# Optimization experiments

Measured on AMD Instinct MI355X. Metric: run time of the kernel, lower is better.

The kernel has to match this reference:

```python
import jax, jax.numpy as jnp
import numpy as np

NUM_EMBED = 204
HEAD_DIM = 64
B, T = 4, 4096


def setup_inputs() -> dict:
    key = jax.random.key(0)
    kx, kq, kk, kv = jax.random.split(key, 4)
    x = jax.random.normal(kx, (B, T, NUM_EMBED), dtype=jnp.float32)
    s = 1.0 / np.sqrt(NUM_EMBED)
    Wq = jax.random.normal(kq, (NUM_EMBED, HEAD_DIM), dtype=jnp.float32) * s
    Wk = jax.random.normal(kk, (NUM_EMBED, HEAD_DIM), dtype=jnp.float32) * s
    Wv = jax.random.normal(kv, (NUM_EMBED, HEAD_DIM), dtype=jnp.float32) * s
    return {"x": x, "Wq": Wq, "Wk": Wk, "Wv": Wv, "mask": True}


def reference(x, Wq, Wk, Wv, mask):
    # Single-head causal attention. d_k = x.shape[-1] (as in the source, which
    # scales by sqrt of the INPUT embed dim, not head_dim).
    Bn, Tn, d_k = x.shape
    q = x @ Wq  # [B,T,H]
    k = x @ Wk  # [B,T,H]
    v = x @ Wv  # [B,T,H]
    scale = 1.0 / jnp.sqrt(jnp.asarray(d_k, dtype=x.dtype))
    scores = jnp.einsum("bqh,bkh->bqk", q, k) * scale  # [B,T,T]
    if mask:
        causal = jnp.tril(jnp.ones((Tn, Tn), dtype=bool))  # allow j <= i
        scores = jnp.where(causal, scores, jnp.finfo(scores.dtype).min)
    attn = jax.nn.softmax(scores, axis=-1)
    out = jnp.einsum("bqk,bkh->bqh", attn, v)  # [B,T,H]
    # dropout is identity in eval mode
    return out
```

## Files before the change

kernel.cpp:

```cpp
#include <hip/hip_runtime.h>

#define TSEQ   4096
#define NB     4
#define EMB    204
#define HD     64
#define WK     224
#define XSTR   232
#define PSTR   68
#define KTILE  64

typedef __attribute__((ext_vector_type(8))) short bf16x8;
typedef __attribute__((ext_vector_type(4))) float f32x4;

__device__ __forceinline__ short f2bf(float f) {
    unsigned u = __float_as_uint(f);
    return (short)((u + 0x7fffu + ((u >> 16) & 1u)) >> 16);
}
__device__ __forceinline__ float bf2f(short h) {
    return __uint_as_float(((unsigned)(unsigned short)h) << 16);
}

__global__ __launch_bounds__(256) void prep_zero_kernel(
    const float* __restrict__ Wq,
    const float* __restrict__ Wk,
    const float* __restrict__ Wv,
    short* __restrict__ Wt,
    float* __restrict__ zacc)
{
    int f = blockIdx.x * 256 + threadIdx.x;
    if (f < 3 * HD * WK) {
        int e   = f % WK;
        int h   = (f / WK) % HD;
        int mat = f / (WK * HD);
        const float* W = (mat == 0) ? Wq : (mat == 1) ? Wk : Wv;
        float v = (e < EMB) ? W[e * HD + h] : 0.f;
        Wt[f] = f2bf(v);
    }
    for (int c = blockIdx.x * 256 + threadIdx.x; c < 266240; c += 256 * 256)
        *(float4*)(zacc + c * 4) = make_float4(0.f, 0.f, 0.f, 0.f);
}

__global__ __launch_bounds__(192) void qkv_mfma_kernel(
    const float* __restrict__ x,
    const short* __restrict__ Wt,
    short* __restrict__ qg,
    short* __restrict__ kg,
    short* __restrict__ vtg)
{
    __shared__ __align__(16) short xs[16 * XSTR];

    const int t    = threadIdx.x;
    const int lane = t & 63;
    const int w    = t >> 6;
    const int l15  = lane & 15;
    const int quad = lane >> 4;
    const long long rowb = (long long)blockIdx.x * 16;

    for (int c = t; c < 816; c += 192) {
        int r = c / 51, c4 = c % 51;
        float4 xv = *(const float4*)(x + (rowb + r) * EMB + c4 * 4);
        unsigned p0 = (unsigned)(unsigned short)f2bf(xv.x)
                    | ((unsigned)(unsigned short)f2bf(xv.y) << 16);
        unsigned p1 = (unsigned)(unsigned short)f2bf(xv.z)
                    | ((unsigned)(unsigned short)f2bf(xv.w) << 16);
        uint2 pk; pk.x = p0; pk.y = p1;
        *(uint2*)(&xs[r * XSTR + c4 * 4]) = pk;
    }
    for (int c = t; c < 16 * 28; c += 192) {
        int r = c / 28, cc = c % 28;
        xs[r * XSTR + EMB + cc] = 0;
    }
    __syncthreads();

    f32x4 acc[4];
#pragma unroll
    for (int nt = 0; nt < 4; ++nt) acc[nt] = (f32x4){0.f, 0.f, 0.f, 0.f};

    const short* Wb = Wt + (size_t)w * HD * WK;
#pragma unroll
    for (int ks = 0; ks < 7; ++ks) {
        bf16x8 af = *(const bf16x8*)(&xs[l15 * XSTR + ks * 32 + quad * 8]);
#pragma unroll
        for (int nt = 0; nt < 4; ++nt) {
            bf16x8 bfr = *(const bf16x8*)(Wb + (size_t)(nt * 16 + l15) * WK
                                          + ks * 32 + quad * 8);
            acc[nt] = __builtin_amdgcn_mfma_f32_16x16x32_bf16(af, bfr, acc[nt], 0, 0, 0);
        }
    }

    const float scale = 0.07001400420f;
    if (w == 0) {
#pragma unroll
        for (int r = 0; r < 4; ++r) {
            long long grow = rowb + quad * 4 + r;
#pragma unroll
            for (int nt = 0; nt < 4; ++nt)
                qg[grow * HD + nt * 16 + l15] = f2bf(acc[nt][r] * scale);
        }
    } else if (w == 1) {
#pragma unroll
        for (int r = 0; r < 4; ++r) {
            long long grow = rowb + quad * 4 + r;
#pragma unroll
            for (int nt = 0; nt < 4; ++nt)
                kg[grow * HD + nt * 16 + l15] = f2bf(acc[nt][r]);
        }
    } else {
#pragma unroll
        for (int r = 0; r < 4; ++r) {
            long long grow = rowb + quad * 4 + r;
            int bb = (int)(grow >> 12);
            int tt = (int)(grow & 4095);
#pragma unroll
            for (int nt = 0; nt < 4; ++nt)
                vtg[((long long)bb * HD + nt * 16 + l15) * TSEQ + tt] = f2bf(acc[nt][r]);
        }
    }
}

__global__ __launch_bounds__(256, 3) void flash_mfma_kernel(
    const short* __restrict__ qg,
    const short* __restrict__ kg,
    const short* __restrict__ vtg,
    float* __restrict__ outacc,
    float* __restrict__ lacc)
{
    __shared__ __align__(16) short Ks[2][KTILE * HD];
    __shared__ __align__(16) short Vt[2][HD * KTILE];
    __shared__ __align__(16) short Ps[4 * 32 * PSTR];

    const int t    = threadIdx.x;
    const int lane = t & 63;
    const int w    = t >> 6;
    const int l15  = lane & 15;
    const int quad = lane >> 4;
    const int wq   = w * 32;

    const int b = blockIdx.y;
    const int p = 143 - (int)blockIdx.x;

    int g = 0;
    while (g < 7 && p >= 2 * (g + 1) * (g + 2)) ++g;
    const int rel    = p - 2 * g * (g + 1);
    const int s      = g + 1;
    const int qt3    = 4 * g + rel / s;
    const int split  = rel % s;
    const int ntiles = 2 * qt3 + 2;
    const int chunk  = (ntiles + s - 1) / s;
    const int kt0    = split * chunk;
    const int kt1    = min(ntiles, kt0 + chunk);
    if (kt0 >= kt1) return;

    const int qbase = qt3 * 128;
    const long long rowb = (long long)b * TSEQ;

    bf16x8 aq[2][2];
#pragma unroll
    for (int m = 0; m < 2; ++m)
#pragma unroll
        for (int ss = 0; ss < 2; ++ss)
            aq[m][ss] = *(const bf16x8*)(qg + (rowb + qbase + wq + m * 16 + l15) * HD
                                         + ss * 32 + quad * 8);

    f32x4 Oacc[2][4];
#pragma unroll
    for (int m = 0; m < 2; ++m)
#pragma unroll
        for (int nt = 0; nt < 4; ++nt) Oacc[m][nt] = (f32x4){0.f, 0.f, 0.f, 0.f};
    float lsum[2][4] = {{0.f, 0.f, 0.f, 0.f}, {0.f, 0.f, 0.f, 0.f}};

    short* pw = &Ps[w * 32 * PSTR];

#define STAGE(BUF, KT) do {                                                   \
        const int k0s = (KT) * KTILE;                                         \
        _Pragma("unroll")                                                     \
        for (int j = 0; j < 2; ++j) {                                         \
            const int rr = (w * 2 + j) * 8 + (lane >> 3);                     \
            const int cc = (lane & 7) ^ (rr & 7);                             \
            const short* srcK = kg + (rowb + k0s + rr) * HD + cc * 8;         \
            __builtin_amdgcn_global_load_lds(                                 \
                (const __attribute__((address_space(1))) void*)srcK,          \
                (__attribute__((address_space(3))) void*)&Ks[BUF][(w * 2 + j) * 512], \
                16, 0, 0);                                                    \
            const short* srcV = vtg + ((long long)b * HD + rr) * TSEQ + k0s + cc * 8; \
            __builtin_amdgcn_global_load_lds(                                 \
                (const __attribute__((address_space(1))) void*)srcV,          \
                (__attribute__((address_space(3))) void*)&Vt[BUF][(w * 2 + j) * 512], \
                16, 0, 0);                                                    \
        }                                                                     \
    } while (0)

    int cur = 0;
    STAGE(0, kt0);
    __syncthreads();

    for (int kt = kt0; kt < kt1; ++kt) {
        const int k0 = kt * KTILE;
        if (kt + 1 < kt1) STAGE(cur ^ 1, kt + 1);

        const short* ksb = Ks[cur];
        const short* vsb = Vt[cur];
        const bool act = (k0 <= qbase + wq);

        if (act) {
#pragma unroll
            for (int m = 0; m < 2; ++m) {
                const int rbase = qbase + wq + m * 16;
                f32x4 S[4];
#pragma unroll
                for (int nt = 0; nt < 4; ++nt) S[nt] = (f32x4){0.f, 0.f, 0.f, 0.f};
#pragma unroll
                for (int ss = 0; ss < 2; ++ss) {
#pragma unroll
                    for (int nt = 0; nt < 4; ++nt) {
                        const int rr = nt * 16 + l15;
                        const int cc = ((ss * 4 + quad) ^ (rr & 7)) * 8;
                        bf16x8 bk = *(const bf16x8*)(ksb + rr * HD + cc);
                        S[nt] = __builtin_amdgcn_mfma_f32_16x16x32_bf16(aq[m][ss], bk, S[nt], 0, 0, 0);
                    }
                }
                if (k0 + 63 <= rbase) {
#pragma unroll
                    for (int r = 0; r < 4; ++r) {
#pragma unroll
                        for (int nt = 0; nt < 4; ++nt) {
                            float pv = __expf(S[nt][r]);
                            short h = f2bf(pv);
                            pw[(m * 16 + quad * 4 + r) * PSTR + nt * 16 + l15] = h;
                            lsum[m][r] += bf2f(h);
                        }
                    }
                } else {
#pragma unroll
                    for (int r = 0; r < 4; ++r) {
                        const int irow = rbase + quad * 4 + r;
#pragma unroll
                        for (int nt = 0; nt < 4; ++nt) {
                            const int j = k0 + nt * 16 + l15;
                            float pv = (j <= irow) ? __expf(S[nt][r]) : 0.f;
                            short h = f2bf(pv);
                            pw[(m * 16 + quad * 4 + r) * PSTR + nt * 16 + l15] = h;
                            lsum[m][r] += bf2f(h);
                        }
                    }
                }
            }

#pragma unroll
            for (int ss = 0; ss < 2; ++ss) {
                bf16x8 pa0 = *(const bf16x8*)(pw + l15 * PSTR + ss * 32 + quad * 8);
                bf16x8 pa1 = *(const bf16x8*)(pw + (16 + l15) * PSTR + ss * 32 + quad * 8);
#pragma unroll
                for (int nt = 0; nt < 4; ++nt) {
                    const int hh = nt * 16 + l15;
                    const int cc = ((ss * 4 + quad) ^ (hh & 7)) * 8;
                    bf16x8 vb = *(const bf16x8*)(vsb + hh * HD + cc);
                    Oacc[0][nt] = __builtin_amdgcn_mfma_f32_16x16x32_bf16(pa0, vb, Oacc[0][nt], 0, 0, 0);
                    Oacc[1][nt] = __builtin_amdgcn_mfma_f32_16x16x32_bf16(pa1, vb, Oacc[1][nt], 0, 0, 0);
                }
            }
        }

        __syncthreads();
        cur ^= 1;
    }

#pragma unroll
    for (int m = 0; m < 2; ++m)
#pragma unroll
        for (int r = 0; r < 4; ++r) {
#pragma unroll
            for (int off = 1; off < 16; off <<= 1)
                lsum[m][r] += __shfl_xor(lsum[m][r], off, 64);
        }

    float* oa = outacc + (rowb + qbase + wq) * HD;
#pragma unroll
    for (int m = 0; m < 2; ++m) {
#pragma unroll
        for (int r = 0; r < 4; ++r) {
            const int row = m * 16 + quad * 4 + r;
#pragma unroll
            for (int nt = 0; nt < 4; ++nt)
                atomicAdd(&oa[row * HD + nt * 16 + l15], Oacc[m][nt][r]);
            if (l15 == 0)
                atomicAdd(&lacc[rowb + qbase + wq + row], lsum[m][r]);
        }
    }
#undef STAGE
}

__global__ __launch_bounds__(256) void finalize_kernel(
    const float* __restrict__ outacc,
    const float* __restrict__ lacc,
    float* __restrict__ out)
{
    int row = blockIdx.x * 16 + (threadIdx.x >> 4);
    int c4  = (threadIdx.x & 15) * 4;
    float inv = 1.0f / lacc[row];
    float4 v = *(const float4*)(outacc + (size_t)row * HD + c4);
    v.x *= inv; v.y *= inv; v.z *= inv; v.w *= inv;
    *(float4*)(out + (size_t)row * HD + c4) = v;
}

extern "C" void kernel_launch(void* const* d_in, const int* in_sizes, int n_in,
                              void* d_out, int out_size, void* d_ws, size_t ws_size,
                              hipStream_t stream)
{
    const float* x  = (const float*)d_in[0];
    const float* Wq = (const float*)d_in[1];
    const float* Wk = (const float*)d_in[2];
    const float* Wv = (const float*)d_in[3];

    const size_t nrows = (size_t)NB * TSEQ;
    short* qg  = (short*)d_ws;
    short* kg  = qg + nrows * HD;
    short* vtg = kg + nrows * HD;
    short* Wt  = vtg + nrows * HD;
    float* outacc = (float*)(Wt + 3 * HD * WK);
    float* lacc   = outacc + nrows * HD;
    float* outp = (float*)d_out;

    prep_zero_kernel<<<dim3(256), dim3(256), 0, stream>>>(Wq, Wk, Wv, Wt, outacc);
    qkv_mfma_kernel<<<dim3(1024), dim3(192), 0, stream>>>(x, Wt, qg, kg, vtg);
    flash_mfma_kernel<<<dim3(144, NB), dim3(256), 0, stream>>>(qg, kg, vtg, outacc, lacc);
    finalize_kernel<<<dim3(1024), dim3(256), 0, stream>>>(outacc, lacc, outp);
}
```

Measured before the change: 123.0 us.

## Switch flash attention to transposed 32x32x16 MFMA with register-resident P

Rewrites the attention inner loop to compute S transposed with 32x32x16 bf16 MFMAs, so the probabilities stay in registers. They are packed with v_cvt_pk_bf16_f32 and rearranged with permlane32_swap instead of going through an LDS staging buffer. Q is prescaled by log2(e)/sqrt(d) so exp2 can replace expf. The work split over query tiles is rebalanced to 272 blocks per batch and the occupancy hint is raised to 4. This removes LDS round-trips and shuffle reductions, at the cost of more atomics per block and heavier register pressure.

```diff
diff --git a/kernel.cpp b/kernel.cpp
--- a/kernel.cpp
+++ b/kernel.cpp
@@ -6,18 +6,16 @@
 #define HD     64
 #define WK     224
 #define XSTR   232
-#define PSTR   68
 #define KTILE  64
 
 typedef __attribute__((ext_vector_type(8))) short bf16x8;
 typedef __attribute__((ext_vector_type(4))) float f32x4;
+typedef __attribute__((ext_vector_type(16))) float f32x16;
+typedef __attribute__((ext_vector_type(4))) unsigned u32x4;
 
 __device__ __forceinline__ short f2bf(float f) {
     unsigned u = __float_as_uint(f);
     return (short)((u + 0x7fffu + ((u >> 16) & 1u)) >> 16);
-}
-__device__ __forceinline__ float bf2f(short h) {
-    return __uint_as_float(((unsigned)(unsigned short)h) << 16);
 }
 
 __global__ __launch_bounds__(256) void prep_zero_kernel(
@@ -88,7 +86,7 @@
         }
     }
 
-    const float scale = 0.07001400420f;
+    const float scale = 0.101008857f;
     if (w == 0) {
 #pragma unroll
         for (int r = 0; r < 4; ++r) {
@@ -118,7 +116,7 @@
     }
 }
 
-__global__ __launch_bounds__(256, 3) void flash_mfma_kernel(
+__global__ __launch_bounds__(256, 4) void flash_mfma_kernel(
     const short* __restrict__ qg,
     const short* __restrict__ kg,
     const short* __restrict__ vtg,
@@ -127,49 +125,45 @@
 {
     __shared__ __align__(16) short Ks[2][KTILE * HD];
     __shared__ __align__(16) short Vt[2][HD * KTILE];
-    __shared__ __align__(16) short Ps[4 * 32 * PSTR];
 
     const int t    = threadIdx.x;
     const int lane = t & 63;
     const int w    = t >> 6;
-    const int l15  = lane & 15;
-    const int quad = lane >> 4;
+    const int l31  = lane & 31;
+    const int hi   = lane >> 5;
     const int wq   = w * 32;
 
     const int b = blockIdx.y;
-    const int p = 143 - (int)blockIdx.x;
-
-    int g = 0;
-    while (g < 7 && p >= 2 * (g + 1) * (g + 2)) ++g;
-    const int rel    = p - 2 * g * (g + 1);
-    const int s      = g + 1;
-    const int qt3    = 4 * g + rel / s;
-    const int split  = rel % s;
+    const int p = 271 - (int)blockIdx.x;
+
+    int qt3 = 0, base = 0;
+    for (;; ++qt3) {
+        int sg = (qt3 + 2) >> 1;
+        if (p < base + sg) break;
+        base += sg;
+    }
+    const int s      = (qt3 + 2) >> 1;
+    const int split  = p - base;
     const int ntiles = 2 * qt3 + 2;
     const int chunk  = (ntiles + s - 1) / s;
     const int kt0    = split * chunk;
     const int kt1    = min(ntiles, kt0 + chunk);
-    if (kt0 >= kt1) return;
 
     const int qbase = qt3 * 128;
     const long long rowb = (long long)b * TSEQ;
-
-    bf16x8 aq[2][2];
-#pragma unroll
-    for (int m = 0; m < 2; ++m)
-#pragma unroll
-        for (int ss = 0; ss < 2; ++ss)
-            aq[m][ss] = *(const bf16x8*)(qg + (rowb + qbase + wq + m * 16 + l15) * HD
-                                         + ss * 32 + quad * 8);
-
-    f32x4 Oacc[2][4];
-#pragma unroll
-    for (int m = 0; m < 2; ++m)
-#pragma unroll
-        for (int nt = 0; nt < 4; ++nt) Oacc[m][nt] = (f32x4){0.f, 0.f, 0.f, 0.f};
-    float lsum[2][4] = {{0.f, 0.f, 0.f, 0.f}, {0.f, 0.f, 0.f, 0.f}};
-
-    short* pw = &Ps[w * 32 * PSTR];
+    const int qA = qbase + wq + l31;
+
+    bf16x8 aq[4];
+#pragma unroll
+    for (int c = 0; c < 4; ++c)
+        aq[c] = *(const bf16x8*)(qg + (rowb + qA) * HD + c * 16 + hi * 8);
+
+    f32x16 Oacc[2];
+#pragma unroll
+    for (int hg = 0; hg < 2; ++hg)
+#pragma unroll
+        for (int r = 0; r < 16; ++r) Oacc[hg][r] = 0.f;
+    float lsum = 0.f;
 
 #define STAGE(BUF, KT) do {                                                   \
         const int k0s = (KT) * KTILE;                                         \
@@ -200,63 +194,53 @@
 
         const short* ksb = Ks[cur];
         const short* vsb = Vt[cur];
-        const bool act = (k0 <= qbase + wq);
+        const bool act  = (k0 <= qbase + wq + 31);
+        const bool full = (k0 + 63 <= qbase + wq);
 
         if (act) {
-#pragma unroll
-            for (int m = 0; m < 2; ++m) {
-                const int rbase = qbase + wq + m * 16;
-                f32x4 S[4];
-#pragma unroll
-                for (int nt = 0; nt < 4; ++nt) S[nt] = (f32x4){0.f, 0.f, 0.f, 0.f};
-#pragma unroll
-                for (int ss = 0; ss < 2; ++ss) {
-#pragma unroll
-                    for (int nt = 0; nt < 4; ++nt) {
-                        const int rr = nt * 16 + l15;
-                        const int cc = ((ss * 4 + quad) ^ (rr & 7)) * 8;
-                        bf16x8 bk = *(const bf16x8*)(ksb + rr * HD + cc);
-                        S[nt] = __builtin_amdgcn_mfma_f32_16x16x32_bf16(aq[m][ss], bk, S[nt], 0, 0, 0);
+            unsigned cd[2][8];
+#pragma unroll
+            for (int kg2 = 0; kg2 < 2; ++kg2) {
+                f32x16 S;
+#pragma unroll
+                for (int r = 0; r < 16; ++r) S[r] = 0.f;
+#pragma unroll
+                for (int c = 0; c < 4; ++c) {
+                    bf16x8 kf = *(const bf16x8*)(ksb + (kg2 * 32 + l31) * HD
+                                   + (((2 * c + hi) ^ (l31 & 7)) * 8));
+                    S = __builtin_amdgcn_mfma_f32_32x32x16_bf16(kf, aq[c], S, 0, 0, 0);
+                }
+                const int jb = k0 + kg2 * 32 + 4 * hi;
+#pragma unroll
+                for (int g = 0; g < 8; ++g) {
+                    float e0 = __builtin_amdgcn_exp2f(S[2 * g]);
+                    float e1 = __builtin_amdgcn_exp2f(S[2 * g + 1]);
+                    if (!full) {
+                        const int j0 = jb + 8 * (g >> 1) + 2 * (g & 1);
+                        if (j0     > qA) e0 = 0.f;
+                        if (j0 + 1 > qA) e1 = 0.f;
                     }
-                }
-                if (k0 + 63 <= rbase) {
-#pragma unroll
-                    for (int r = 0; r < 4; ++r) {
-#pragma unroll
-                        for (int nt = 0; nt < 4; ++nt) {
-                            float pv = __expf(S[nt][r]);
-                            short h = f2bf(pv);
-                            pw[(m * 16 + quad * 4 + r) * PSTR + nt * 16 + l15] = h;
-                            lsum[m][r] += bf2f(h);
-                        }
-                    }
-                } else {
-#pragma unroll
-                    for (int r = 0; r < 4; ++r) {
-                        const int irow = rbase + quad * 4 + r;
-#pragma unroll
-                        for (int nt = 0; nt < 4; ++nt) {
-                            const int j = k0 + nt * 16 + l15;
-                            float pv = (j <= irow) ? __expf(S[nt][r]) : 0.f;
-                            short h = f2bf(pv);
-                            pw[(m * 16 + quad * 4 + r) * PSTR + nt * 16 + l15] = h;
-                            lsum[m][r] += bf2f(h);
-                        }
-                    }
+                    lsum += e0 + e1;
+                    asm("v_cvt_pk_bf16_f32 %0, %1, %2"
+                        : "=v"(cd[kg2][g]) : "v"(e0), "v"(e1));
                 }
             }
 
 #pragma unroll
-            for (int ss = 0; ss < 2; ++ss) {
-                bf16x8 pa0 = *(const bf16x8*)(pw + l15 * PSTR + ss * 32 + quad * 8);
-                bf16x8 pa1 = *(const bf16x8*)(pw + (16 + l15) * PSTR + ss * 32 + quad * 8);
-#pragma unroll
-                for (int nt = 0; nt < 4; ++nt) {
-                    const int hh = nt * 16 + l15;
-                    const int cc = ((ss * 4 + quad) ^ (hh & 7)) * 8;
-                    bf16x8 vb = *(const bf16x8*)(vsb + hh * HD + cc);
-                    Oacc[0][nt] = __builtin_amdgcn_mfma_f32_16x16x32_bf16(pa0, vb, Oacc[0][nt], 0, 0, 0);
-                    Oacc[1][nt] = __builtin_amdgcn_mfma_f32_16x16x32_bf16(pa1, vb, Oacc[1][nt], 0, 0, 0);
+            for (int kc = 0; kc < 4; ++kc) {
+                unsigned u0 = cd[kc >> 1][4 * (kc & 1) + 0];
+                unsigned u1 = cd[kc >> 1][4 * (kc & 1) + 1];
+                unsigned u2 = cd[kc >> 1][4 * (kc & 1) + 2];
+                unsigned u3 = cd[kc >> 1][4 * (kc & 1) + 3];
+                asm("v_permlane32_swap_b32 %0, %1" : "+v"(u0), "+v"(u2));
+                asm("v_permlane32_swap_b32 %0, %1" : "+v"(u1), "+v"(u3));
+                u32x4 pk = {u0, u1, u2, u3};
+                bf16x8 pb = __builtin_bit_cast(bf16x8, pk);
+#pragma unroll
+                for (int hg = 0; hg < 2; ++hg) {
+                    bf16x8 vf = *(const bf16x8*)(vsb + (hg * 32 + l31) * HD
+                                   + (((2 * kc + hi) ^ (l31 & 7)) * 8));
+                    Oacc[hg] = __builtin_amdgcn_mfma_f32_32x32x16_bf16(vf, pb, Oacc[hg], 0, 0, 0);
                 }
             }
         }
@@ -265,28 +249,16 @@
         cur ^= 1;
     }
 
-#pragma unroll
-    for (int m = 0; m < 2; ++m)
-#pragma unroll
-        for (int r = 0; r < 4; ++r) {
-#pragma unroll
-            for (int off = 1; off < 16; off <<= 1)
-                lsum[m][r] += __shfl_xor(lsum[m][r], off, 64);
-        }
-
-    float* oa = outacc + (rowb + qbase + wq) * HD;
-#pragma unroll
-    for (int m = 0; m < 2; ++m) {
-#pragma unroll
-        for (int r = 0; r < 4; ++r) {
-            const int row = m * 16 + quad * 4 + r;
-#pragma unroll
-            for (int nt = 0; nt < 4; ++nt)
-                atomicAdd(&oa[row * HD + nt * 16 + l15], Oacc[m][nt][r]);
-            if (l15 == 0)
-                atomicAdd(&lacc[rowb + qbase + wq + row], lsum[m][r]);
-        }
-    }
+    lsum += __shfl_xor(lsum, 32, 64);
+
+    float* oa = outacc + (rowb + qA) * HD;
+#pragma unroll
+    for (int hg = 0; hg < 2; ++hg)
+#pragma unroll
+        for (int r = 0; r < 16; ++r)
+            atomicAdd(&oa[hg * 32 + 4 * hi + (r & 3) + 8 * (r >> 2)], Oacc[hg][r]);
+    if (hi == 0)
+        atomicAdd(&lacc[rowb + qA], lsum);
 #undef STAGE
 }
 
@@ -323,6 +295,6 @@
 
     prep_zero_kernel<<<dim3(256), dim3(256), 0, stream>>>(Wq, Wk, Wv, Wt, outacc);
     qkv_mfma_kernel<<<dim3(1024), dim3(192), 0, stream>>>(x, Wt, qg, kg, vtg);
-    flash_mfma_kernel<<<dim3(144, NB), dim3(256), 0, stream>>>(qg, kg, vtg, outacc, lacc);
+    flash_mfma_kernel<<<dim3(272, NB), dim3(256), 0, stream>>>(qg, kg, vtg, outacc, lacc);
     finalize_kernel<<<dim3(1024), dim3(256), 0, stream>>>(outacc, lacc, outp);
 }
```

After: 312.8 us. 154% more time.
